# Kernel optimization log

Hardware: AMD Instinct MI355X
Metric: run time of the kernel (lower is better)

Reference implementation:

```python
import jax, jax.numpy as jnp
import numpy as np
from jax import lax

NUM_CLASSES = 10
NUM_ITER = 3
DN = ('NCHW', 'OIHW', 'NCHW')


def squash(t, axis=-1):
    sq = (t ** 2).sum(axis=axis, keepdims=True)
    return (sq / (1.0 + sq)) * t / jnp.sqrt(sq)


def setup_inputs() -> dict:
    key = jax.random.key(0)
    ks = jax.random.split(key, 12)
    B = 512
    s = 0.05  # param scale for numerical stability
    return {
        'x': jax.random.normal(ks[0], (B, 1, 28, 28), jnp.float32),
        'conv1_w': jax.random.normal(ks[1], (256, 1, 9, 9), jnp.float32) * s,
        'conv1_b': jax.random.normal(ks[2], (256,), jnp.float32) * s,
        'prim_w': jax.random.normal(ks[3], (8, 32, 256, 9, 9), jnp.float32) * s,
        'prim_b': jax.random.normal(ks[4], (8, 32), jnp.float32) * s,
        'route_w': jax.random.normal(ks[5], (NUM_CLASSES, 32 * 6 * 6, 8, 16), jnp.float32),
        'dec_w1': jax.random.normal(ks[6], (512, 16 * NUM_CLASSES), jnp.float32) * s,
        'dec_b1': jax.random.normal(ks[7], (512,), jnp.float32) * s,
        'dec_w2': jax.random.normal(ks[8], (1024, 512), jnp.float32) * s,
        'dec_b2': jax.random.normal(ks[9], (1024,), jnp.float32) * s,
        'dec_w3': jax.random.normal(ks[10], (784, 1024), jnp.float32) * s,
        'dec_b3': jax.random.normal(ks[11], (784,), jnp.float32) * s,
    }


def reference(x, conv1_w, conv1_b, prim_w, prim_b, route_w,
              dec_w1, dec_b1, dec_w2, dec_b2, dec_w3, dec_b3):
    B = x.shape[0]
    # conv1 + relu: [B,256,20,20]
    h = lax.conv_general_dilated(x, conv1_w, (1, 1), 'VALID', dimension_numbers=DN)
    h = jax.nn.relu(h + conv1_b[None, :, None, None])
    # primary capsules: 8 parallel convs fused into one conv with 8*32 out channels
    kw = prim_w.reshape(8 * 32, 256, 9, 9)
    u = lax.conv_general_dilated(h, kw, (2, 2), 'VALID', dimension_numbers=DN)
    u = u + prim_b.reshape(-1)[None, :, None, None]          # [B,256,6,6]
    u = u.reshape(B, 8, 32 * 6 * 6).transpose(0, 2, 1)       # [B,1152,8]
    u = squash(u, axis=-1)
    # digit capsules: priors [C,B,R,16]
    priors = jnp.einsum('bri,crio->cbro', u, route_w)
    logits = jnp.zeros_like(priors)
    for i in range(NUM_ITER):
        probs = jax.nn.softmax(logits, axis=2)
        v = squash((probs * priors).sum(axis=2, keepdims=True))  # [C,B,1,16]
        if i != NUM_ITER - 1:
            logits = logits + (priors * v).sum(axis=-1, keepdims=True)
    caps = v.squeeze(2).transpose(1, 0, 2)                    # [B,C,16]
    classes = jnp.sqrt((caps ** 2).sum(axis=-1))              # [B,C]
    classes = jax.nn.softmax(classes, axis=1)
    y = jax.nn.one_hot(jnp.argmax(classes, axis=1), NUM_CLASSES, dtype=caps.dtype)
    d = (caps * y[:, :, None]).reshape(B, -1)                 # [B,160]
    d = jax.nn.relu(d @ dec_w1.T + dec_b1)
    d = jax.nn.relu(d @ dec_w2.T + dec_b2)
    recon = jax.nn.sigmoid(d @ dec_w3.T + dec_b3)             # [B,784]
    return classes, recon
```

## Files before the change

kernel.cpp:

```cpp
#include <hip/hip_runtime.h>
#include <math.h>


typedef _Float16 f16;
typedef _Float16 f16x8 __attribute__((ext_vector_type(8)));
typedef _Float16 f16x4 __attribute__((ext_vector_type(4)));
typedef float f32x4 __attribute__((ext_vector_type(4)));

__device__ __forceinline__ void gl_lds16(const void* g, void* l) {
  __builtin_amdgcn_global_load_lds(
      (const __attribute__((address_space(1))) void*)g,
      (__attribute__((address_space(3))) void*)l, 16, 0, 0);
}

__global__ __launch_bounds__(256, 2) void conv1_kernel(
    const float* __restrict__ x, const float* __restrict__ w,
    const float* __restrict__ bias, f16* __restrict__ ht)
{
  __shared__ float xs[784];
  const int b = blockIdx.x;
  const int t = threadIdx.x;
  for (int i = t; i < 784; i += 256) xs[i] = x[b * 784 + i];
  float wr[81];
#pragma unroll
  for (int k = 0; k < 81; ++k) wr[k] = w[t * 81 + k];
  const float bv = bias[t];
  __syncthreads();
  for (int oy = 0; oy < 20; ++oy) {
    float acc[20];
#pragma unroll
    for (int i = 0; i < 20; ++i) acc[i] = bv;
#pragma unroll
    for (int ky = 0; ky < 9; ++ky) {
      float xr[28];
#pragma unroll
      for (int q = 0; q < 7; ++q) {
        const float4 v = *(const float4*)&xs[(oy + ky) * 28 + q * 4];
        xr[q*4+0] = v.x; xr[q*4+1] = v.y; xr[q*4+2] = v.z; xr[q*4+3] = v.w;
      }
#pragma unroll
      for (int kx = 0; kx < 9; ++kx) {
        const float wv = wr[ky * 9 + kx];
#pragma unroll
        for (int ox = 0; ox < 20; ++ox) acc[ox] = fmaf(xr[ox + kx], wv, acc[ox]);
      }
    }
    f16* hp = &ht[(size_t)((b * 20 + oy) * 20) * 256 + t];
#pragma unroll
    for (int ox = 0; ox < 20; ++ox)
      hp[ox * 256] = (f16)fmaxf(acc[ox], 0.f);
  }
}

__global__ __launch_bounds__(256) void wtrans_kernel(
    const float* __restrict__ w, f16* __restrict__ wt)
{
  __shared__ float tile[64 * 83];
  const int oc = blockIdx.x;
  const int icq = blockIdx.y;
  const int t = threadIdx.x;
  const float* src = w + (size_t)oc * 20736 + (size_t)icq * 64 * 81;
  for (int idx = t; idx < 5184; idx += 256) {
    const int ici = idx / 81, kk = idx - ici * 81;
    tile[ici * 83 + kk] = src[idx];
  }
  __syncthreads();
  f16* dst = wt + (size_t)oc * 20736 + icq * 64;
  for (int idx = t; idx < 5184; idx += 256) {
    const int kk = idx >> 6, ici = idx & 63;
    dst[kk * 256 + ici] = (f16)tile[ici * 83 + kk];
  }
}

__global__ __launch_bounds__(256) void prim_mfma_kernel(
    const f16* __restrict__ ht, const f16* __restrict__ wt,
    float* __restrict__ part)
{
  __shared__ f16 sm[8192];
  const int t = threadIdx.x;
  const int wv = t >> 6, lane = t & 63;
  const int id = blockIdx.x;
  const int g = id >> 3;
  const int mb = (id & 7) + 8 * (g >> 2);
  const int nb = (g >> 1) & 1;
  const int ks = g & 1;
  const int m0 = mb * 128, n0 = nb * 128;

  const int chunk = (lane & 3) ^ ((lane >> 3) & 3);
  long aoff[2], boff[2];
#pragma unroll
  for (int i = 0; i < 2; ++i) {
    const int r = wv * 32 + i * 16 + (lane >> 2);
    const int m = m0 + r;
    const int b = m / 36, pos = m - b * 36;
    const int oy = pos / 6, ox = pos - oy * 6;
    aoff[i] = (long)(((b * 20 + 2 * oy) * 20 + 2 * ox) * 256) * 2 + chunk * 16;
    boff[i] = (long)(n0 + r) * 41472 + chunk * 16;
  }
  const char* htc = (const char*)ht;
  const char* wtc = (const char*)wt;

  const int lrow = lane & 15, quad = lane >> 4;
  const int qx = quad ^ ((lrow >> 1) & 3);
  const int wm = wv & 1, wn = wv >> 1;
  f32x4 acc[4][4] = {};

  const int s0 = ks * 324, s1 = s0 + 324;
  for (int s = s0; s < s1; ++s) {
    const int kykx = s >> 3, icb = s & 7;
    const int ky = kykx / 9, kx = kykx - ky * 9;
    const long astep = (long)((((ky * 20 + kx) * 256) + icb * 32) * 2);
    const long bstep = (long)(((kykx * 256) + icb * 32) * 2);
    __syncthreads();
    {
      char* dA = (char*)sm + wv * 2048;
      char* dB = (char*)sm + 8192 + wv * 2048;
      gl_lds16(htc + aoff[0] + astep, dA);
      gl_lds16(htc + aoff[1] + astep, dA + 1024);
      gl_lds16(wtc + boff[0] + bstep, dB);
      gl_lds16(wtc + boff[1] + bstep, dB + 1024);
    }
    __syncthreads();
    const f16* As = sm;
    const f16* Bs = sm + 4096;
    f16x8 af[4], bf[4];
#pragma unroll
    for (int mt = 0; mt < 4; ++mt)
      af[mt] = *(const f16x8*)&As[(wm * 64 + mt * 16 + lrow) * 32 + qx * 8];
#pragma unroll
    for (int nt = 0; nt < 4; ++nt)
      bf[nt] = *(const f16x8*)&Bs[(wn * 64 + nt * 16 + lrow) * 32 + qx * 8];
#pragma unroll
    for (int mt = 0; mt < 4; ++mt)
#pragma unroll
      for (int nt = 0; nt < 4; ++nt)
        acc[mt][nt] = __builtin_amdgcn_mfma_f32_16x16x32_f16(
            af[mt], bf[nt], acc[mt][nt], 0, 0, 0);
  }

  float* pp = part + (size_t)ks * 4718592;
#pragma unroll
  for (int mt = 0; mt < 4; ++mt) {
    const int mbase = m0 + wm * 64 + mt * 16 + quad * 4;
#pragma unroll
    for (int nt = 0; nt < 4; ++nt) {
      const int n = n0 + wn * 64 + nt * 16 + lrow;
      const int np = (n & 31) * 8 + (n >> 5);
#pragma unroll
      for (int rg = 0; rg < 4; ++rg)
        pp[(size_t)(mbase + rg) * 256 + np] = acc[mt][nt][rg];
    }
  }
}

__global__ void squash_kernel(const float* __restrict__ part,
                              const float* __restrict__ bias,
                              float* __restrict__ u)
{
  const int tid = blockIdx.x * 256 + threadIdx.x;
  if (tid >= 512 * 36 * 32) return;
  const int cc = tid & 31;
  const int row = tid >> 5;
  const int b = row / 36;
  const int pos = row - b * 36;
  const float* p = part + (size_t)row * 256 + cc * 8;
  float v[8] = {};
#pragma unroll
  for (int ksl = 0; ksl < 2; ++ksl) {
    const float4 a0 = *(const float4*)(p + (size_t)ksl * 4718592);
    const float4 a1 = *(const float4*)(p + (size_t)ksl * 4718592 + 4);
    v[0] += a0.x; v[1] += a0.y; v[2] += a0.z; v[3] += a0.w;
    v[4] += a1.x; v[5] += a1.y; v[6] += a1.z; v[7] += a1.w;
  }
  float sq = 0.f;
#pragma unroll
  for (int i = 0; i < 8; ++i) {
    v[i] += bias[i * 32 + cc];
    sq = fmaf(v[i], v[i], sq);
  }
  const float scale = sq / ((1.f + sq) * sqrtf(sq));
  float* up = &u[(size_t)(b * 1152 + cc * 36 + pos) * 8];
#pragma unroll
  for (int i = 0; i < 8; ++i) up[i] = v[i] * scale;
}

__global__ __launch_bounds__(256, 4) void priors_kernel(
    const float* __restrict__ u, const float* __restrict__ rw,
    f16* __restrict__ P)
{
  const int t = threadIdx.x;
  const int rl = t >> 2, oq = t & 3;
  const int r = blockIdx.x * 64 + rl;
  const int b0 = blockIdx.y * 64;
  const int c = blockIdx.z;

  float4 wreg[8];
  const float* wbase = rw + (size_t)(c * 1152 + r) * 128 + oq * 4;
#pragma unroll
  for (int k = 0; k < 8; ++k)
    wreg[k] = *(const float4*)(wbase + k * 16);

  f16* pbase = P + (size_t)((c * 512 + b0) * 1152 + r) * 16 + oq * 4;
  const float* ubase = u + (size_t)(b0 * 1152 + r) * 8;

  for (int b = 0; b < 64; ++b) {
    const float4 ua = *(const float4*)(ubase + (size_t)b * 9216);
    const float4 ub = *(const float4*)(ubase + (size_t)b * 9216 + 4);
    const float uu[8] = {ua.x, ua.y, ua.z, ua.w, ub.x, ub.y, ub.z, ub.w};
    float ax = 0.f, ay = 0.f, az = 0.f, aw = 0.f;
#pragma unroll
    for (int k = 0; k < 8; ++k) {
      ax = fmaf(uu[k], wreg[k].x, ax);
      ay = fmaf(uu[k], wreg[k].y, ay);
      az = fmaf(uu[k], wreg[k].z, az);
      aw = fmaf(uu[k], wreg[k].w, aw);
    }
    f16x4 st;
    st[0] = (f16)ax; st[1] = (f16)ay; st[2] = (f16)az; st[3] = (f16)aw;
    *(f16x4*)(pbase + (size_t)b * 18432) = st;
  }
}

__device__ __forceinline__ float wave_sum(float v) {
#pragma unroll
  for (int off = 32; off > 0; off >>= 1) v += __shfl_xor(v, off);
  return v;
}
__device__ __forceinline__ float wave_max(float v) {
#pragma unroll
  for (int off = 32; off > 0; off >>= 1) v = fmaxf(v, __shfl_xor(v, off));
  return v;
}

__global__ __launch_bounds__(256, 2) void routing_kernel(
    const f16* __restrict__ Pg, float* __restrict__ caps)
{
  const int c = blockIdx.x >> 9;
  const int b = blockIdx.x & 511;
  const int t = threadIdx.x;
  const int wid = t >> 6;
  const int lane = t & 63;
  __shared__ float xred[4 * 17];

  float P[5][16];
  float lg[5];
  const int nk = (t < 128) ? 5 : 4;
#pragma unroll
  for (int k = 0; k < 5; ++k)
#pragma unroll
    for (int o = 0; o < 16; ++o) P[k][o] = 0.f;

  const f16* pbase = Pg + (size_t)((c * 512 + b) * 1152) * 16;
#pragma unroll
  for (int k = 0; k < 5; ++k) {
    if (k < nk) {
      const int r = t + (k << 8);
      const f16x8 p0 = *(const f16x8*)&pbase[(size_t)r * 16];
      const f16x8 p1 = *(const f16x8*)&pbase[(size_t)r * 16 + 8];
#pragma unroll
      for (int o = 0; o < 8; ++o) {
        P[k][o]     = (float)p0[o];
        P[k][o + 8] = (float)p1[o];
      }
    }
  }

  float v[16];
  {
    float sq = 0.f;
#pragma unroll
    for (int o = 0; o < 16; ++o) {
      float p = 0.f;
#pragma unroll
      for (int k = 0; k < 5; ++k) p += P[k][o];
      p = wave_sum(p);
      if (lane == 0) xred[wid * 17 + o] = p;
      v[o] = 0.f;
    }
    __syncthreads();
#pragma unroll
    for (int o = 0; o < 16; ++o) {
      const float s = (xred[o] + xred[17 + o] + xred[34 + o] + xred[51 + o]) *
                      (1.f / 1152.f);
      v[o] = s;
      sq = fmaf(s, s, sq);
    }
    const float scale = sq / ((1.f + sq) * sqrtf(sq));
#pragma unroll
    for (int o = 0; o < 16; ++o) v[o] *= scale;
    __syncthreads();
  }
#pragma unroll
  for (int k = 0; k < 5; ++k) {
    float a = 0.f;
#pragma unroll
    for (int o = 0; o < 16; ++o) a = fmaf(P[k][o], v[o], a);
    lg[k] = a;
  }

  for (int it = 1; it < 3; ++it) {
    float m = -1e30f;
#pragma unroll
    for (int k = 0; k < 5; ++k) if (k < nk) m = fmaxf(m, lg[k]);
    m = wave_max(m);
    if (lane == 0) xred[wid * 17 + 16] = m;
    __syncthreads();
    const float mx = fmaxf(fmaxf(xred[16], xred[17 + 16]),
                           fmaxf(xred[34 + 16], xred[51 + 16]));
    __syncthreads();
    float e[5];
#pragma unroll
    for (int k = 0; k < 5; ++k) e[k] = (k < nk) ? expf(lg[k] - mx) : 0.f;
    float pS = 0.f;
#pragma unroll
    for (int k = 0; k < 5; ++k) pS += e[k];
    pS = wave_sum(pS);
    if (lane == 0) xred[wid * 17 + 16] = pS;
#pragma unroll
    for (int o = 0; o < 16; ++o) {
      float p = 0.f;
#pragma unroll
      for (int k = 0; k < 5; ++k) p = fmaf(e[k], P[k][o], p);
      p = wave_sum(p);
      if (lane == 0) xred[wid * 17 + o] = p;
    }
    __syncthreads();
    const float S = xred[16] + xred[17 + 16] + xred[34 + 16] + xred[51 + 16];
    const float inv = 1.f / S;
    float sq = 0.f;
#pragma unroll
    for (int o = 0; o < 16; ++o) {
      const float s = (xred[o] + xred[17 + o] + xred[34 + o] + xred[51 + o]) * inv;
      v[o] = s;
      sq = fmaf(s, s, sq);
    }
    const float scale = sq / ((1.f + sq) * sqrtf(sq));
#pragma unroll
    for (int o = 0; o < 16; ++o) v[o] *= scale;
    __syncthreads();
    if (it < 2) {
#pragma unroll
      for (int k = 0; k < 5; ++k) {
        float a = 0.f;
#pragma unroll
        for (int o = 0; o < 16; ++o) a = fmaf(P[k][o], v[o], a);
        lg[k] += a;
      }
    }
  }
  if (t == 0) {
    float* cp = &caps[(b * 10 + c) * 16];
#pragma unroll
    for (int o = 0; o < 16; ++o) cp[o] = v[o];
  }
}

__global__ void classes_kernel(const float* __restrict__ caps,
                               float* __restrict__ out_classes,
                               float* __restrict__ d0)
{
  const int b = blockIdx.x * 256 + threadIdx.x;
  if (b >= 512) return;
  float nrm[10];
#pragma unroll
  for (int cc = 0; cc < 10; ++cc) {
    float sq = 0.f;
#pragma unroll
    for (int o = 0; o < 16; ++o) {
      const float vv = caps[(b * 10 + cc) * 16 + o];
      sq = fmaf(vv, vv, sq);
    }
    nrm[cc] = sqrtf(sq);
  }
  float mx = nrm[0]; int cs = 0;
#pragma unroll
  for (int cc = 1; cc < 10; ++cc)
    if (nrm[cc] > mx) { mx = nrm[cc]; cs = cc; }
  float e[10], ssum = 0.f;
#pragma unroll
  for (int cc = 0; cc < 10; ++cc) { e[cc] = expf(nrm[cc] - mx); ssum += e[cc]; }
  const float inv = 1.f / ssum;
#pragma unroll
  for (int cc = 0; cc < 10; ++cc) out_classes[b * 10 + cc] = e[cc] * inv;
#pragma unroll
  for (int cc = 0; cc < 10; ++cc)
#pragma unroll
    for (int o = 0; o < 16; ++o)
      d0[b * 160 + cc * 16 + o] = (cc == cs) ? caps[(b * 10 + cc) * 16 + o] : 0.f;
}

__global__ __launch_bounds__(256, 2) void fc_kernel(
    const float* __restrict__ A, const float* __restrict__ W,
    const float* __restrict__ bias, float* __restrict__ C,
    int N, int K, int act)
{
  __shared__ float As[64][17];
  __shared__ float Ws[64][17];
  const int t = threadIdx.x;
  const int tm = t >> 4, tn = t & 15;
  const int m0 = blockIdx.y << 6, n0 = blockIdx.x << 6;
  const int lr = t >> 2, lq = (t & 3) << 2;
  float acc[4][4] = {};
  for (int k0 = 0; k0 < K; k0 += 16) {
    const float4 av = *(const float4*)&A[(m0 + lr) * K + k0 + lq];
    float4 wv = make_float4(0.f, 0.f, 0.f, 0.f);
    const int wn = n0 + lr;
    if (wn < N) wv = *(const float4*)&W[wn * K + k0 + lq];
    __syncthreads();
    As[lr][lq+0] = av.x; As[lr][lq+1] = av.y; As[lr][lq+2] = av.z; As[lr][lq+3] = av.w;
    Ws[lr][lq+0] = wv.x; Ws[lr][lq+1] = wv.y; Ws[lr][lq+2] = wv.z; Ws[lr][lq+3] = wv.w;
    __syncthreads();
#pragma unroll
    for (int kk = 0; kk < 16; ++kk) {
      float a[4], w[4];
#pragma unroll
      for (int i = 0; i < 4; ++i) a[i] = As[tm * 4 + i][kk];
#pragma unroll
      for (int j = 0; j < 4; ++j) w[j] = Ws[tn * 4 + j][kk];
#pragma unroll
      for (int i = 0; i < 4; ++i)
#pragma unroll
        for (int j = 0; j < 4; ++j) acc[i][j] = fmaf(a[i], w[j], acc[i][j]);
    }
  }
#pragma unroll
  for (int i = 0; i < 4; ++i) {
    const int m = m0 + tm * 4 + i;
#pragma unroll
    for (int j = 0; j < 4; ++j) {
      const int n = n0 + tn * 4 + j;
      if (n < N) {
        float vv = acc[i][j] + bias[n];
        vv = act ? (1.f / (1.f + expf(-vv))) : fmaxf(vv, 0.f);
        C[m * N + n] = vv;
      }
    }
  }
}

extern "C" void kernel_launch(void* const* d_in, const int* in_sizes, int n_in,
                              void* d_out, int out_size, void* d_ws, size_t ws_size,
                              hipStream_t stream)
{
  const float* x       = (const float*)d_in[0];
  const float* conv1_w = (const float*)d_in[1];
  const float* conv1_b = (const float*)d_in[2];
  const float* prim_w  = (const float*)d_in[3];
  const float* prim_b  = (const float*)d_in[4];
  const float* route_w = (const float*)d_in[5];
  const float* dec_w1  = (const float*)d_in[6];
  const float* dec_b1  = (const float*)d_in[7];
  const float* dec_w2  = (const float*)d_in[8];
  const float* dec_b2  = (const float*)d_in[9];
  const float* dec_w3  = (const float*)d_in[10];
  const float* dec_b3  = (const float*)d_in[11];
  float* out = (float*)d_out;

  char* ws = (char*)d_ws;
  f16*   ht   = (f16*)(ws);
  f16*   wtp  = (f16*)(ws + 104857600);
  float* part = (float*)(ws + 115474432);
  float* u    = (float*)(ws + 188743680);
  f16*   P    = (f16*)(ws);
  float* caps = (float*)(ws + 207618048);
  float* d0   = (float*)(ws + 207945728);
  float* d1   = (float*)(ws + 208273408);
  float* d2   = (float*)(ws + 209321984);

  hipLaunchKernelGGL(conv1_kernel, dim3(512), dim3(256), 0, stream,
                     x, conv1_w, conv1_b, ht);
  hipLaunchKernelGGL(wtrans_kernel, dim3(256, 4), dim3(256), 0, stream,
                     prim_w, wtp);
  hipLaunchKernelGGL(prim_mfma_kernel, dim3(576), dim3(256), 0, stream,
                     ht, wtp, part);
  hipLaunchKernelGGL(squash_kernel, dim3(2304), dim3(256), 0, stream,
                     part, prim_b, u);
  hipLaunchKernelGGL(priors_kernel, dim3(18, 8, 10), dim3(256), 0, stream,
                     u, route_w, P);
  hipLaunchKernelGGL(routing_kernel, dim3(5120), dim3(256), 0, stream,
                     P, caps);
  hipLaunchKernelGGL(classes_kernel, dim3(2), dim3(256), 0, stream,
                     caps, out, d0);
  hipLaunchKernelGGL(fc_kernel, dim3(8, 8), dim3(256), 0, stream,
                     d0, dec_w1, dec_b1, d1, 512, 160, 0);
  hipLaunchKernelGGL(fc_kernel, dim3(16, 8), dim3(256), 0, stream,
                     d1, dec_w2, dec_b2, d2, 1024, 512, 0);
  hipLaunchKernelGGL(fc_kernel, dim3(13, 8), dim3(256), 0, stream,
                     d2, dec_w3, dec_b3, out + 5120, 784, 1024, 1);
}
```

Before: 826.2 us.

## Split conv1 rows across blocks, raise prim split-K to four, fuse decoder MLP

Conv1 now launches four blocks per image, each computing five output rows, so there are more blocks to fill the GPU. The primary-capsule MFMA GEMM splits K four ways instead of two, doubling the grid, and squash sums four partial slices. The three decoder FC launches become one fused kernel that processes four rows per block and keeps intermediates in LDS. In exchange, partial-sum traffic grows, conv1 weights are reloaded by each row-group block, and the fused decoder has only 128 blocks, each streaming the full weight matrices.

```diff
diff --git a/kernel.cpp b/kernel.cpp
--- a/kernel.cpp
+++ b/kernel.cpp
@@ -17,16 +17,17 @@
     const float* __restrict__ x, const float* __restrict__ w,
     const float* __restrict__ bias, f16* __restrict__ ht)
 {
-  __shared__ float xs[784];
+  __shared__ float xs[364];
   const int b = blockIdx.x;
+  const int y0 = blockIdx.y * 5;
   const int t = threadIdx.x;
-  for (int i = t; i < 784; i += 256) xs[i] = x[b * 784 + i];
+  for (int i = t; i < 364; i += 256) xs[i] = x[b * 784 + y0 * 28 + i];
   float wr[81];
 #pragma unroll
   for (int k = 0; k < 81; ++k) wr[k] = w[t * 81 + k];
   const float bv = bias[t];
   __syncthreads();
-  for (int oy = 0; oy < 20; ++oy) {
+  for (int oy = y0; oy < y0 + 5; ++oy) {
     float acc[20];
 #pragma unroll
     for (int i = 0; i < 20; ++i) acc[i] = bv;
@@ -35,7 +36,7 @@
       float xr[28];
 #pragma unroll
       for (int q = 0; q < 7; ++q) {
-        const float4 v = *(const float4*)&xs[(oy + ky) * 28 + q * 4];
+        const float4 v = *(const float4*)&xs[(oy - y0 + ky) * 28 + q * 4];
         xr[q*4+0] = v.x; xr[q*4+1] = v.y; xr[q*4+2] = v.z; xr[q*4+3] = v.w;
       }
 #pragma unroll
@@ -81,9 +82,9 @@
   const int wv = t >> 6, lane = t & 63;
   const int id = blockIdx.x;
   const int g = id >> 3;
-  const int mb = (id & 7) + 8 * (g >> 2);
-  const int nb = (g >> 1) & 1;
-  const int ks = g & 1;
+  const int ks = g & 3;
+  const int nb = (g >> 2) & 1;
+  const int mb = (id & 7) + 8 * (g >> 3);
   const int m0 = mb * 128, n0 = nb * 128;
 
   const int chunk = (lane & 3) ^ ((lane >> 3) & 3);
@@ -105,7 +106,7 @@
   const int wm = wv & 1, wn = wv >> 1;
   f32x4 acc[4][4] = {};
 
-  const int s0 = ks * 324, s1 = s0 + 324;
+  const int s0 = ks * 162, s1 = s0 + 162;
   for (int s = s0; s < s1; ++s) {
     const int kykx = s >> 3, icb = s & 7;
     const int ky = kykx / 9, kx = kykx - ky * 9;
@@ -166,7 +167,7 @@
   const float* p = part + (size_t)row * 256 + cc * 8;
   float v[8] = {};
 #pragma unroll
-  for (int ksl = 0; ksl < 2; ++ksl) {
+  for (int ksl = 0; ksl < 4; ++ksl) {
     const float4 a0 = *(const float4*)(p + (size_t)ksl * 4718592);
     const float4 a1 = *(const float4*)(p + (size_t)ksl * 4718592 + 4);
     v[0] += a0.x; v[1] += a0.y; v[2] += a0.z; v[3] += a0.w;
@@ -389,52 +390,92 @@
       d0[b * 160 + cc * 16 + o] = (cc == cs) ? caps[(b * 10 + cc) * 16 + o] : 0.f;
 }
 
-__global__ __launch_bounds__(256, 2) void fc_kernel(
-    const float* __restrict__ A, const float* __restrict__ W,
-    const float* __restrict__ bias, float* __restrict__ C,
-    int N, int K, int act)
-{
-  __shared__ float As[64][17];
-  __shared__ float Ws[64][17];
+__global__ __launch_bounds__(256, 2) void decoder_kernel(
+    const float* __restrict__ d0,
+    const float* __restrict__ W1, const float* __restrict__ b1,
+    const float* __restrict__ W2, const float* __restrict__ b2,
+    const float* __restrict__ W3, const float* __restrict__ b3,
+    float* __restrict__ recon)
+{
+  __shared__ float s0[4 * 160];
+  __shared__ float s1[4 * 512];
+  __shared__ float s2[4 * 1024];
   const int t = threadIdx.x;
-  const int tm = t >> 4, tn = t & 15;
-  const int m0 = blockIdx.y << 6, n0 = blockIdx.x << 6;
-  const int lr = t >> 2, lq = (t & 3) << 2;
-  float acc[4][4] = {};
-  for (int k0 = 0; k0 < K; k0 += 16) {
-    const float4 av = *(const float4*)&A[(m0 + lr) * K + k0 + lq];
-    float4 wv = make_float4(0.f, 0.f, 0.f, 0.f);
-    const int wn = n0 + lr;
-    if (wn < N) wv = *(const float4*)&W[wn * K + k0 + lq];
-    __syncthreads();
-    As[lr][lq+0] = av.x; As[lr][lq+1] = av.y; As[lr][lq+2] = av.z; As[lr][lq+3] = av.w;
-    Ws[lr][lq+0] = wv.x; Ws[lr][lq+1] = wv.y; Ws[lr][lq+2] = wv.z; Ws[lr][lq+3] = wv.w;
-    __syncthreads();
-#pragma unroll
-    for (int kk = 0; kk < 16; ++kk) {
-      float a[4], w[4];
-#pragma unroll
-      for (int i = 0; i < 4; ++i) a[i] = As[tm * 4 + i][kk];
-#pragma unroll
-      for (int j = 0; j < 4; ++j) w[j] = Ws[tn * 4 + j][kk];
-#pragma unroll
-      for (int i = 0; i < 4; ++i)
-#pragma unroll
-        for (int j = 0; j < 4; ++j) acc[i][j] = fmaf(a[i], w[j], acc[i][j]);
-    }
-  }
-#pragma unroll
-  for (int i = 0; i < 4; ++i) {
-    const int m = m0 + tm * 4 + i;
-#pragma unroll
-    for (int j = 0; j < 4; ++j) {
-      const int n = n0 + tn * 4 + j;
-      if (n < N) {
-        float vv = acc[i][j] + bias[n];
-        vv = act ? (1.f / (1.f + expf(-vv))) : fmaxf(vv, 0.f);
-        C[m * N + n] = vv;
-      }
-    }
+  const int row0 = blockIdx.x * 4;
+
+  for (int i = t; i < 640; i += 256) {
+    const int r = i / 160, k = i - r * 160;
+    s0[i] = d0[(row0 + r) * 160 + k];
+  }
+  __syncthreads();
+
+#pragma unroll
+  for (int j = 0; j < 2; ++j) {
+    const int n = t + j * 256;
+    float a0 = 0.f, a1 = 0.f, a2 = 0.f, a3 = 0.f;
+    const float* wr = &W1[n * 160];
+    for (int k = 0; k < 160; k += 4) {
+      const float4 w = *(const float4*)&wr[k];
+#pragma unroll
+      for (int q = 0; q < 4; ++q) {
+        const float wq = (&w.x)[q];
+        a0 = fmaf(s0[k + q],       wq, a0);
+        a1 = fmaf(s0[160 + k + q], wq, a1);
+        a2 = fmaf(s0[320 + k + q], wq, a2);
+        a3 = fmaf(s0[480 + k + q], wq, a3);
+      }
+    }
+    const float bb = b1[n];
+    s1[n]        = fmaxf(a0 + bb, 0.f);
+    s1[512 + n]  = fmaxf(a1 + bb, 0.f);
+    s1[1024 + n] = fmaxf(a2 + bb, 0.f);
+    s1[1536 + n] = fmaxf(a3 + bb, 0.f);
+  }
+  __syncthreads();
+
+#pragma unroll
+  for (int j = 0; j < 4; ++j) {
+    const int n = t + j * 256;
+    float a0 = 0.f, a1 = 0.f, a2 = 0.f, a3 = 0.f;
+    const float* wr = &W2[n * 512];
+    for (int k = 0; k < 512; k += 4) {
+      const float4 w = *(const float4*)&wr[k];
+#pragma unroll
+      for (int q = 0; q < 4; ++q) {
+        const float wq = (&w.x)[q];
+        a0 = fmaf(s1[k + q],        wq, a0);
+        a1 = fmaf(s1[512 + k + q],  wq, a1);
+        a2 = fmaf(s1[1024 + k + q], wq, a2);
+        a3 = fmaf(s1[1536 + k + q], wq, a3);
+      }
+    }
+    const float bb = b2[n];
+    s2[n]        = fmaxf(a0 + bb, 0.f);
+    s2[1024 + n] = fmaxf(a1 + bb, 0.f);
+    s2[2048 + n] = fmaxf(a2 + bb, 0.f);
+    s2[3072 + n] = fmaxf(a3 + bb, 0.f);
+  }
+  __syncthreads();
+
+  for (int n = t; n < 784; n += 256) {
+    float a0 = 0.f, a1 = 0.f, a2 = 0.f, a3 = 0.f;
+    const float* wr = &W3[n * 1024];
+    for (int k = 0; k < 1024; k += 4) {
+      const float4 w = *(const float4*)&wr[k];
+#pragma unroll
+      for (int q = 0; q < 4; ++q) {
+        const float wq = (&w.x)[q];
+        a0 = fmaf(s2[k + q],        wq, a0);
+        a1 = fmaf(s2[1024 + k + q], wq, a1);
+        a2 = fmaf(s2[2048 + k + q], wq, a2);
+        a3 = fmaf(s2[3072 + k + q], wq, a3);
+      }
+    }
+    const float bb = b3[n];
+    recon[(row0 + 0) * 784 + n] = 1.f / (1.f + expf(-(a0 + bb)));
+    recon[(row0 + 1) * 784 + n] = 1.f / (1.f + expf(-(a1 + bb)));
+    recon[(row0 + 2) * 784 + n] = 1.f / (1.f + expf(-(a2 + bb)));
+    recon[(row0 + 3) * 784 + n] = 1.f / (1.f + expf(-(a3 + bb)));
   }
 }
 
@@ -460,18 +501,16 @@
   f16*   ht   = (f16*)(ws);
   f16*   wtp  = (f16*)(ws + 104857600);
   float* part = (float*)(ws + 115474432);
-  float* u    = (float*)(ws + 188743680);
+  float* u    = (float*)(ws + 190971904);
   f16*   P    = (f16*)(ws);
-  float* caps = (float*)(ws + 207618048);
-  float* d0   = (float*)(ws + 207945728);
-  float* d1   = (float*)(ws + 208273408);
-  float* d2   = (float*)(ws + 209321984);
-
-  hipLaunchKernelGGL(conv1_kernel, dim3(512), dim3(256), 0, stream,
+  float* caps = (float*)(ws + 209846272);
+  float* d0   = (float*)(ws + 210173952);
+
+  hipLaunchKernelGGL(conv1_kernel, dim3(512, 4), dim3(256), 0, stream,
                      x, conv1_w, conv1_b, ht);
   hipLaunchKernelGGL(wtrans_kernel, dim3(256, 4), dim3(256), 0, stream,
                      prim_w, wtp);
-  hipLaunchKernelGGL(prim_mfma_kernel, dim3(576), dim3(256), 0, stream,
+  hipLaunchKernelGGL(prim_mfma_kernel, dim3(1152), dim3(256), 0, stream,
                      ht, wtp, part);
   hipLaunchKernelGGL(squash_kernel, dim3(2304), dim3(256), 0, stream,
                      part, prim_b, u);
@@ -481,10 +520,7 @@
                      P, caps);
   hipLaunchKernelGGL(classes_kernel, dim3(2), dim3(256), 0, stream,
                      caps, out, d0);
-  hipLaunchKernelGGL(fc_kernel, dim3(8, 8), dim3(256), 0, stream,
-                     d0, dec_w1, dec_b1, d1, 512, 160, 0);
-  hipLaunchKernelGGL(fc_kernel, dim3(16, 8), dim3(256), 0, stream,
-                     d1, dec_w2, dec_b2, d2, 1024, 512, 0);
-  hipLaunchKernelGGL(fc_kernel, dim3(13, 8), dim3(256), 0, stream,
-                     d2, dec_w3, dec_b3, out + 5120, 784, 1024, 1);
-}
+  hipLaunchKernelGGL(decoder_kernel, dim3(128), dim3(256), 0, stream,
+                     d0, dec_w1, dec_b1, dec_w2, dec_b2, dec_w3, dec_b3,
+                     out + 5120);
+}
```

New measurement: 954.3 us. 15.5% more time.
